# Performance work log

Hardware: AMD Instinct MI355X
Metric: run time of the kernel (lower is better)

The kernel has to match this reference:

```python
import jax, jax.numpy as jnp
import numpy as np

BS, SL, NC = 512, 1024, 64


def setup_inputs() -> dict:
    key = jax.random.key(0)
    k1, k2, k3, k4 = jax.random.split(key, 4)
    inputs = jax.random.normal(k1, (BS, SL, NC), dtype=jnp.float32)
    # valid-suffix padding masks: True = padded position (as in the torch module)
    lengths = jax.random.randint(k2, (BS,), SL // 2, SL + 1)
    masks = jnp.arange(SL)[None, :] >= lengths[:, None]  # bool [BS, SL]
    tag_indices = jax.random.randint(k3, (BS, SL), 0, NC).astype(jnp.int64)
    transitions = jax.random.normal(k4, (NC, NC), dtype=jnp.float32) * 0.01
    return {"inputs": inputs, "masks": masks, "tag_indices": tag_indices,
            "transitions": transitions}


def _crf_loss(inputs, masks, tag_indices, transitions):
    bs, sl, nc = inputs.shape
    # unary score: emission at gold tag per step, padded steps zeroed
    unary = jnp.take_along_axis(inputs, tag_indices[..., None], axis=2)[..., 0]
    unary = jnp.where(masks, 0.0, unary).sum(axis=1)  # [bs]
    # binary score: transition between consecutive gold tags
    binary = transitions[tag_indices[:, :-1], tag_indices[:, 1:]]  # [bs, sl-1]
    binary = jnp.where(masks[:, 1:], 0.0, binary).sum(axis=1)  # [bs]
    # log partition via forward algorithm (lax.scan over time)
    def step(alphas, xs):
        x_t, m_t = xs  # [bs, nc], [bs]
        scores = alphas[:, :, None] + transitions[None, :, :]  # [bs, nc(from), nc(to)]
        new_alphas = x_t + jax.nn.logsumexp(scores, axis=1)
        alphas = jnp.where(m_t[:, None], alphas, new_alphas)
        return alphas, None

    xs = (jnp.swapaxes(inputs[:, 1:, :], 0, 1), jnp.swapaxes(masks[:, 1:], 0, 1))
    alphas, _ = jax.lax.scan(step, inputs[:, 0, :], xs)
    log_norm = jax.nn.logsumexp(alphas, axis=1)  # [bs]
    log_likelihood = unary + binary - log_norm
    loss = jnp.sum(-log_likelihood) / bs  # batch_average=True
    return loss


def reference(inputs, masks, tag_indices, transitions):
    loss = _crf_loss(inputs, masks, tag_indices, transitions)
    return (loss, transitions)
```

## Files before the change

### kernel.cpp

```cpp
#include <hip/hip_runtime.h>

#define BS 512
#define SL 1024
#define NC 64

template <int CTRL>
__device__ __forceinline__ float dppf(float x) {
    return __int_as_float(__builtin_amdgcn_mov_dpp(__float_as_int(x), CTRL, 0xF, 0xF, true));
}
__device__ __forceinline__ float rflf(float x) {
    return __int_as_float(__builtin_amdgcn_readfirstlane(__float_as_int(x)));
}

__device__ __forceinline__ void halfswap32(float x, float& r0, float& r1) {
#if __has_builtin(__builtin_amdgcn_permlane32_swap)
    auto r = __builtin_amdgcn_permlane32_swap(__float_as_int(x), __float_as_int(x), false, false);
    r0 = __int_as_float(r[0]); r1 = __int_as_float(r[1]);
#else
    float w = __shfl_xor(x, 32, 64);
    bool up = (threadIdx.x & 32) != 0;
    r0 = up ? w : x;
    r1 = up ? x : w;
#endif
}
__device__ __forceinline__ void halfswap16(float x, float& r0, float& r1) {
#if __has_builtin(__builtin_amdgcn_permlane16_swap)
    auto r = __builtin_amdgcn_permlane16_swap(__float_as_int(x), __float_as_int(x), false, false);
    r0 = __int_as_float(r[0]); r1 = __int_as_float(r[1]);
#else
    float w = __int_as_float(__builtin_amdgcn_ds_swizzle(__float_as_int(x), 0x401F));
    bool up = (threadIdx.x & 16) != 0;
    r0 = up ? w : x;
    r1 = up ? x : w;
#endif
}

__device__ __forceinline__ float wave_sum(float x) {
    x += dppf<0xB1>(x);
    x += dppf<0x4E>(x);
    x += dppf<0x141>(x);
    x += dppf<0x140>(x);
    float a, c;
    halfswap16(x, a, c); x = a + c;
    halfswap32(x, a, c); x = a + c;
    return x;
}

__global__ __launch_bounds__(256) void crf_init_out(const float* __restrict__ trans,
                                                    float* __restrict__ out) {
    int idx = blockIdx.x * 256 + threadIdx.x;
    if (idx == 0) out[0] = 0.0f;
    if (idx < NC * NC) out[1 + idx] = trans[idx];
}

__global__ __launch_bounds__(64, 1) void crf_fwd(const float* __restrict__ inputs,
                                                 const int* __restrict__ masks,
                                                 const int* __restrict__ tags,
                                                 const float* __restrict__ trans,
                                                 float* __restrict__ out) {
    const int b = blockIdx.x;
    const int lane = threadIdx.x;

    __shared__ float Tlds[NC * NC];
    __shared__ int   taglds[SL];

    const float* __restrict__ inrow = inputs + (size_t)b * SL * NC;

#pragma unroll
    for (int i = 0; i < NC; ++i) Tlds[i * NC + lane] = trans[i * NC + lane];

    int len = 0;
#pragma unroll
    for (int k = 0; k < SL / NC; ++k) {
        int idx = k * NC + lane;
        taglds[idx] = tags[(size_t)b * SL + idx];
        unsigned long long bal = __ballot(masks[(size_t)b * SL + idx] == 0);
        len += __popcll(bal);
    }
    __syncthreads();

    int B[4];
    {
        float pf = __int_as_float(lane);
        float p0, p1, a0, a1, c0, c1;
        halfswap32(pf, p0, p1);
        halfswap16(p0, a0, a1);
        halfswap16(p1, c0, c1);
        B[0] = __builtin_amdgcn_readfirstlane(__float_as_int(a0));
        B[1] = __builtin_amdgcn_readfirstlane(__float_as_int(a1));
        B[2] = __builtin_amdgcn_readfirstlane(__float_as_int(c0));
        B[3] = __builtin_amdgcn_readfirstlane(__float_as_int(c1));
    }

    float E[64];
#pragma unroll
    for (int f = 0; f < 4; ++f) {
#pragma unroll
        for (int m = 0; m < 16; ++m) {
            int row = B[f] + ((lane ^ m) & 15);
            E[f * 16 + m] = __expf(Tlds[row * NC + lane]);
        }
    }

    float x0 = inrow[lane];
    float base = rflf(x0);
    float q = __expf(x0 - base);
    int tagprev = taglds[0];
    float u = (lane == tagprev) ? x0 : 0.0f;
    float bacc = 0.0f;

    int   tg_cur = taglds[1];
    float x_cur = inrow[NC + lane];
    float x_n1  = inrow[2 * NC + lane];
    float ex_cur = __expf(x_cur);

    for (int t = 1; t < len; ++t) {
        int t2 = t + 2; if (t2 > SL - 1) t2 = SL - 1;
        float x_n2 = inrow[(size_t)t2 * NC + lane];
        int tn = t + 1; if (tn > SL - 1) tn = SL - 1;
        int tg_next = taglds[tn];
        float Tv = Tlds[tagprev * NC + tg_cur];
        float ex_n1 = __expf(x_n1);

        float m  = rflf(q);
        float rm = __builtin_amdgcn_rcpf(m);
        float ex_eff = ex_cur * rm;
        base += __logf(m);

        float v[64];
        {
            float u0, u1;
            halfswap32(q, u0, u1);
            halfswap16(u0, v[0],  v[16]);
            halfswap16(u1, v[32], v[48]);
#pragma unroll
            for (int F = 0; F < 64; F += 16) {
                v[F + 1]  = dppf<0xB1>(v[F + 0]);
                v[F + 2]  = dppf<0x4E>(v[F + 0]);
                v[F + 3]  = dppf<0x4E>(v[F + 1]);
                v[F + 7]  = dppf<0x141>(v[F + 0]);
                v[F + 6]  = dppf<0x141>(v[F + 1]);
                v[F + 5]  = dppf<0x141>(v[F + 2]);
                v[F + 4]  = dppf<0x141>(v[F + 3]);
                v[F + 15] = dppf<0x140>(v[F + 0]);
                v[F + 14] = dppf<0x140>(v[F + 1]);
                v[F + 13] = dppf<0x140>(v[F + 2]);
                v[F + 12] = dppf<0x140>(v[F + 3]);
                v[F + 11] = dppf<0x140>(v[F + 4]);
                v[F + 10] = dppf<0x140>(v[F + 5]);
                v[F + 9]  = dppf<0x140>(v[F + 6]);
                v[F + 8]  = dppf<0x140>(v[F + 7]);
            }
        }

        float acc0 = 0.f, acc1 = 0.f, acc2 = 0.f, acc3 = 0.f;
        float acc4 = 0.f, acc5 = 0.f, acc6 = 0.f, acc7 = 0.f;
#pragma unroll
        for (int j = 0; j < 64; j += 8) {
            acc0 = fmaf(v[j + 0], E[j + 0], acc0);
            acc1 = fmaf(v[j + 1], E[j + 1], acc1);
            acc2 = fmaf(v[j + 2], E[j + 2], acc2);
            acc3 = fmaf(v[j + 3], E[j + 3], acc3);
            acc4 = fmaf(v[j + 4], E[j + 4], acc4);
            acc5 = fmaf(v[j + 5], E[j + 5], acc5);
            acc6 = fmaf(v[j + 6], E[j + 6], acc6);
            acc7 = fmaf(v[j + 7], E[j + 7], acc7);
        }
        float s = ((acc0 + acc1) + (acc2 + acc3)) + ((acc4 + acc5) + (acc6 + acc7));

        u += (lane == tg_cur) ? x_cur : 0.0f;
        bacc += Tv;

        q = s * ex_eff;

        tagprev = tg_cur; tg_cur = tg_next;
        x_cur = x_n1; x_n1 = x_n2; ex_cur = ex_n1;
    }

    float qsum = wave_sum(q);
    float usum = wave_sum(u);
    float log_norm = base + __logf(qsum);

    if (lane == 0) {
        float ll = usum + bacc - log_norm;
        atomicAdd(out, -ll * (1.0f / BS));
    }
}

extern "C" void kernel_launch(void* const* d_in, const int* in_sizes, int n_in,
                              void* d_out, int out_size, void* d_ws, size_t ws_size,
                              hipStream_t stream) {
    const float* inputs = (const float*)d_in[0];
    const int*   masks  = (const int*)d_in[1];
    const int*   tags   = (const int*)d_in[2];
    const float* trans  = (const float*)d_in[3];
    float* out = (float*)d_out;

    crf_init_out<<<(1 + NC * NC + 255) / 256, 256, 0, stream>>>(trans, out);
    crf_fwd<<<BS, 64, 0, stream>>>(inputs, masks, tags, trans, out);
}
```

Before: 592.3 us.

## Split unary/binary score into separate parallel kernel and slim forward recurrence loop

Moves the gold-path unary and binary score computation out of the serial forward recurrence into a separate 256-thread-per-batch kernel that sums in parallel and atomically adds its contribution. The forward kernel drops the LDS staging of transitions and tags, reads transitions directly from global memory, and interleaves DPP shuffles with FMAs in the 64-way dot product instead of building a 64-entry v array first. The intent is to shorten the per-step critical path and cut register pressure in the latency-bound scan. The cost is an extra kernel launch and a second pass over the tags and masks.

```diff
diff --git a/kernel.cpp b/kernel.cpp
--- a/kernel.cpp
+++ b/kernel.cpp
@@ -53,31 +53,53 @@
     if (idx < NC * NC) out[1 + idx] = trans[idx];
 }
 
-__global__ __launch_bounds__(64, 1) void crf_fwd(const float* __restrict__ inputs,
-                                                 const int* __restrict__ masks,
-                                                 const int* __restrict__ tags,
-                                                 const float* __restrict__ trans,
-                                                 float* __restrict__ out) {
+__global__ __launch_bounds__(256) void crf_ub(const float* __restrict__ inputs,
+                                              const int* __restrict__ masks,
+                                              const int* __restrict__ tags,
+                                              const float* __restrict__ trans,
+                                              float* __restrict__ out) {
+    const int b = blockIdx.x;
+    const int tid = threadIdx.x;
+    const int* tg = tags + (size_t)b * SL;
+    const int* mk = masks + (size_t)b * SL;
+    const float* xb = inputs + (size_t)b * SL * NC;
+
+    float acc = 0.0f;
+    const int t0 = tid * 4;
+    int tprev = (t0 > 0) ? tg[t0 - 1] : 0;
+#pragma unroll
+    for (int j = 0; j < 4; ++j) {
+        int t = t0 + j;
+        int tgt = tg[t];
+        if (mk[t] == 0) {
+            acc += xb[(size_t)t * NC + tgt];
+            if (t > 0) acc += trans[tprev * NC + tgt];
+        }
+        tprev = tgt;
+    }
+
+    acc = wave_sum(acc);
+    __shared__ float r[4];
+    if ((tid & 63) == 0) r[tid >> 6] = acc;
+    __syncthreads();
+    if (tid == 0) atomicAdd(out, -(r[0] + r[1] + r[2] + r[3]) * (1.0f / BS));
+}
+
+__global__ __launch_bounds__(64) __attribute__((amdgpu_waves_per_eu(1)))
+void crf_fwd(const float* __restrict__ inputs,
+             const int* __restrict__ masks,
+             const float* __restrict__ trans,
+             float* __restrict__ out) {
     const int b = blockIdx.x;
     const int lane = threadIdx.x;
-
-    __shared__ float Tlds[NC * NC];
-    __shared__ int   taglds[SL];
-
-    const float* __restrict__ inrow = inputs + (size_t)b * SL * NC;
-
-#pragma unroll
-    for (int i = 0; i < NC; ++i) Tlds[i * NC + lane] = trans[i * NC + lane];
+    const float* __restrict__ xp = inputs + (size_t)b * SL * NC;
 
     int len = 0;
 #pragma unroll
     for (int k = 0; k < SL / NC; ++k) {
-        int idx = k * NC + lane;
-        taglds[idx] = tags[(size_t)b * SL + idx];
-        unsigned long long bal = __ballot(masks[(size_t)b * SL + idx] == 0);
+        unsigned long long bal = __ballot(masks[(size_t)b * SL + k * NC + lane] == 0);
         len += __popcll(bal);
     }
-    __syncthreads();
 
     int B[4];
     {
@@ -98,93 +120,82 @@
 #pragma unroll
         for (int m = 0; m < 16; ++m) {
             int row = B[f] + ((lane ^ m) & 15);
-            E[f * 16 + m] = __expf(Tlds[row * NC + lane]);
+            E[f * 16 + m] = __expf(trans[row * NC + lane]);
         }
     }
-
-    float x0 = inrow[lane];
+#pragma unroll
+    for (int i = 0; i < 64; ++i) {
+        asm volatile("" : "+v"(E[i]));
+    }
+
+    float x0 = xp[lane];
     float base = rflf(x0);
     float q = __expf(x0 - base);
-    int tagprev = taglds[0];
-    float u = (lane == tagprev) ? x0 : 0.0f;
-    float bacc = 0.0f;
-
-    int   tg_cur = taglds[1];
-    float x_cur = inrow[NC + lane];
-    float x_n1  = inrow[2 * NC + lane];
-    float ex_cur = __expf(x_cur);
+
+    float ex  = __expf(xp[NC + lane]);
+    float xn1 = xp[2 * NC + lane];
+    float xn2 = xp[3 * NC + lane];
 
     for (int t = 1; t < len; ++t) {
-        int t2 = t + 2; if (t2 > SL - 1) t2 = SL - 1;
-        float x_n2 = inrow[(size_t)t2 * NC + lane];
-        int tn = t + 1; if (tn > SL - 1) tn = SL - 1;
-        int tg_next = taglds[tn];
-        float Tv = Tlds[tagprev * NC + tg_cur];
-        float ex_n1 = __expf(x_n1);
+        int t3 = t + 3; if (t3 > SL - 1) t3 = SL - 1;
+        float xnew = xp[(size_t)t3 * NC + lane];
+        float exn = __expf(xn1);
 
         float m  = rflf(q);
         float rm = __builtin_amdgcn_rcpf(m);
-        float ex_eff = ex_cur * rm;
+        float ex_eff = ex * rm;
         base += __logf(m);
 
-        float v[64];
-        {
-            float u0, u1;
-            halfswap32(q, u0, u1);
-            halfswap16(u0, v[0],  v[16]);
-            halfswap16(u1, v[32], v[48]);
-#pragma unroll
-            for (int F = 0; F < 64; F += 16) {
-                v[F + 1]  = dppf<0xB1>(v[F + 0]);
-                v[F + 2]  = dppf<0x4E>(v[F + 0]);
-                v[F + 3]  = dppf<0x4E>(v[F + 1]);
-                v[F + 7]  = dppf<0x141>(v[F + 0]);
-                v[F + 6]  = dppf<0x141>(v[F + 1]);
-                v[F + 5]  = dppf<0x141>(v[F + 2]);
-                v[F + 4]  = dppf<0x141>(v[F + 3]);
-                v[F + 15] = dppf<0x140>(v[F + 0]);
-                v[F + 14] = dppf<0x140>(v[F + 1]);
-                v[F + 13] = dppf<0x140>(v[F + 2]);
-                v[F + 12] = dppf<0x140>(v[F + 3]);
-                v[F + 11] = dppf<0x140>(v[F + 4]);
-                v[F + 10] = dppf<0x140>(v[F + 5]);
-                v[F + 9]  = dppf<0x140>(v[F + 6]);
-                v[F + 8]  = dppf<0x140>(v[F + 7]);
-            }
+        float h0, h1, h2, h3, u0, u1;
+        halfswap32(q, u0, u1);
+        halfswap16(u0, h0, h1);
+        halfswap16(u1, h2, h3);
+        float a0 = 0.f, a1 = 0.f, a2 = 0.f, a3 = 0.f;
+        float a4 = 0.f, a5 = 0.f, a6 = 0.f, a7 = 0.f;
+#pragma unroll
+        for (int f = 0; f < 4; ++f) {
+            float v0 = (f == 0) ? h0 : (f == 1) ? h1 : (f == 2) ? h2 : h3;
+            float v1  = dppf<0xB1>(v0);
+            float v2  = dppf<0x4E>(v0);
+            float v3  = dppf<0x4E>(v1);
+            float v7  = dppf<0x141>(v0);
+            float v6  = dppf<0x141>(v1);
+            float v5  = dppf<0x141>(v2);
+            float v4  = dppf<0x141>(v3);
+            a0 = fmaf(v0, E[f * 16 + 0], a0);
+            a1 = fmaf(v1, E[f * 16 + 1], a1);
+            a2 = fmaf(v2, E[f * 16 + 2], a2);
+            a3 = fmaf(v3, E[f * 16 + 3], a3);
+            float v15 = dppf<0x140>(v0);
+            float v14 = dppf<0x140>(v1);
+            float v13 = dppf<0x140>(v2);
+            float v12 = dppf<0x140>(v3);
+            a4 = fmaf(v4, E[f * 16 + 4], a4);
+            a5 = fmaf(v5, E[f * 16 + 5], a5);
+            a6 = fmaf(v6, E[f * 16 + 6], a6);
+            a7 = fmaf(v7, E[f * 16 + 7], a7);
+            float v11 = dppf<0x140>(v4);
+            float v10 = dppf<0x140>(v5);
+            float v9  = dppf<0x140>(v6);
+            float v8  = dppf<0x140>(v7);
+            a0 = fmaf(v8,  E[f * 16 + 8],  a0);
+            a1 = fmaf(v9,  E[f * 16 + 9],  a1);
+            a2 = fmaf(v10, E[f * 16 + 10], a2);
+            a3 = fmaf(v11, E[f * 16 + 11], a3);
+            a4 = fmaf(v12, E[f * 16 + 12], a4);
+            a5 = fmaf(v13, E[f * 16 + 13], a5);
+            a6 = fmaf(v14, E[f * 16 + 14], a6);
+            a7 = fmaf(v15, E[f * 16 + 15], a7);
         }
-
-        float acc0 = 0.f, acc1 = 0.f, acc2 = 0.f, acc3 = 0.f;
-        float acc4 = 0.f, acc5 = 0.f, acc6 = 0.f, acc7 = 0.f;
-#pragma unroll
-        for (int j = 0; j < 64; j += 8) {
-            acc0 = fmaf(v[j + 0], E[j + 0], acc0);
-            acc1 = fmaf(v[j + 1], E[j + 1], acc1);
-            acc2 = fmaf(v[j + 2], E[j + 2], acc2);
-            acc3 = fmaf(v[j + 3], E[j + 3], acc3);
-            acc4 = fmaf(v[j + 4], E[j + 4], acc4);
-            acc5 = fmaf(v[j + 5], E[j + 5], acc5);
-            acc6 = fmaf(v[j + 6], E[j + 6], acc6);
-            acc7 = fmaf(v[j + 7], E[j + 7], acc7);
-        }
-        float s = ((acc0 + acc1) + (acc2 + acc3)) + ((acc4 + acc5) + (acc6 + acc7));
-
-        u += (lane == tg_cur) ? x_cur : 0.0f;
-        bacc += Tv;
-
+        float s = ((a0 + a1) + (a2 + a3)) + ((a4 + a5) + (a6 + a7));
         q = s * ex_eff;
 
-        tagprev = tg_cur; tg_cur = tg_next;
-        x_cur = x_n1; x_n1 = x_n2; ex_cur = ex_n1;
+        ex = exn; xn1 = xn2; xn2 = xnew;
     }
 
     float qsum = wave_sum(q);
-    float usum = wave_sum(u);
     float log_norm = base + __logf(qsum);
-
-    if (lane == 0) {
-        float ll = usum + bacc - log_norm;
-        atomicAdd(out, -ll * (1.0f / BS));
-    }
+    if (lane == 0) atomicAdd(out, log_norm * (1.0f / BS));
 }
 
 extern "C" void kernel_launch(void* const* d_in, const int* in_sizes, int n_in,
@@ -197,5 +208,6 @@
     float* out = (float*)d_out;
 
     crf_init_out<<<(1 + NC * NC + 255) / 256, 256, 0, stream>>>(trans, out);
-    crf_fwd<<<BS, 64, 0, stream>>>(inputs, masks, tags, trans, out);
-}
+    crf_ub<<<BS, 256, 0, stream>>>(inputs, masks, tags, trans, out);
+    crf_fwd<<<BS, 64, 0, stream>>>(inputs, masks, trans, out);
+}
```

Result: no change. 597.7 us (+0.9%).
